# Optimization experiments

Measured on AMD Instinct MI355X. Metric: run time of the kernel, lower is better.

## Reference

```python
import jax, jax.numpy as jnp
import numpy as np
import math

B, T, D = 2, 2048, 2048
H, DH = 16, 128
DKV, DQ, DR = 512, 1024, 64
ROPE_BASE = 500000.0
EPS = 1e-6
SCALE = 1.0 / math.sqrt(DH + DR)


def setup_inputs() -> dict:
    key = jax.random.key(0)
    ks = jax.random.split(key, 12)
    s = 0.02
    return {
        'x': jax.random.normal(ks[0], (B, T, D), jnp.float32),
        'W_DQ': jax.random.normal(ks[1], (D, DQ), jnp.float32) * s,
        'W_UQ': jax.random.normal(ks[2], (DQ, H * DH), jnp.float32) * s,
        'W_QR': jax.random.normal(ks[3], (DQ, H * DR), jnp.float32) * s,
        'W_DKV': jax.random.normal(ks[4], (D, DKV), jnp.float32) * s,
        'W_UK': jax.random.normal(ks[5], (DKV, H * DH), jnp.float32) * s,
        'W_UV': jax.random.normal(ks[6], (DKV, H * DH), jnp.float32) * s,
        'W_KR': jax.random.normal(ks[7], (D, DR), jnp.float32) * s,
        'W_O': jax.random.normal(ks[8], (H * DH, D), jnp.float32) * s,
        'q_norm_w': jnp.ones((DQ,), jnp.float32),
        'kv_norm_w': jnp.ones((DKV,), jnp.float32),
    }


def _rmsnorm(v, w):
    n = jax.lax.rsqrt(jnp.mean(v * v, axis=-1, keepdims=True) + EPS)
    return v * n * w


def _rotate_half(v):
    v1, v2 = jnp.split(v, 2, axis=-1)
    return jnp.concatenate([-v2, v1], axis=-1)


def _rope_tables(seq_len):
    inv_freq = 1.0 / (ROPE_BASE ** (jnp.arange(0, DR, 2, dtype=jnp.float32) / DR))
    t = jnp.arange(seq_len, dtype=jnp.float32)
    freqs = jnp.outer(t, inv_freq)              # (S, DR/2)
    emb = jnp.concatenate([freqs, freqs], -1)   # (S, DR)
    return jnp.cos(emb), jnp.sin(emb)


def reference(x, W_DQ, W_UQ, W_QR, W_DKV, W_UK, W_UV, W_KR, W_O, q_norm_w, kv_norm_w):
    # Query path: low-rank compress -> RMSNorm -> up-project (content + rope parts)
    c_Q = _rmsnorm(x @ W_DQ, q_norm_w)                               # (B,T,DQ)
    q_C = (c_Q @ W_UQ).reshape(B, T, H, DH).transpose(0, 2, 1, 3)    # (B,H,T,DH)
    q_R = (c_Q @ W_QR).reshape(B, T, H, DR).transpose(0, 2, 1, 3)    # (B,H,T,DR)
    # KV path: joint low-rank latent + decoupled rope key
    c_KV = _rmsnorm(x @ W_DKV, kv_norm_w)                            # (B,T,DKV)
    k_C = (c_KV @ W_UK).reshape(B, T, H, DH).transpose(0, 2, 1, 3)   # (B,H,T,DH)
    v_C = (c_KV @ W_UV).reshape(B, T, H, DH).transpose(0, 2, 1, 3)   # (B,H,T,DH)
    k_R = (x @ W_KR)[:, None, :, :]                                  # (B,1,T,DR) shared across heads
    # Decoupled RoPE
    cos, sin = _rope_tables(T)
    cos = cos[None, None]; sin = sin[None, None]                     # (1,1,T,DR)
    q_R = q_R * cos + _rotate_half(q_R) * sin
    k_R = k_R * cos + _rotate_half(k_R) * sin
    k_R = jnp.broadcast_to(k_R, (B, H, T, DR))
    q = jnp.concatenate([q_C, q_R], axis=-1)                         # (B,H,T,DH+DR)
    k = jnp.concatenate([k_C, k_R], axis=-1)
    # Causal attention with MLA scale 1/sqrt(d_head + d_rope)
    scores = jnp.einsum('bhqd,bhkd->bhqk', q, k) * SCALE
    causal = jnp.tril(jnp.ones((T, T), bool))
    scores = jnp.where(causal, scores, jnp.finfo(scores.dtype).min)
    attn = jax.nn.softmax(scores, axis=-1)
    out = jnp.einsum('bhqk,bhkd->bhqd', attn, v_C)                   # (B,H,T,DH)
    out = out.transpose(0, 2, 1, 3).reshape(B, T, H * DH)
    return out @ W_O                                                 # (B,T,D)
```

## Files before the change

### kernel.cpp

```cpp
#include <hip/hip_runtime.h>
#include <cstdint>
#include <cstddef>

#define B_   2
#define T_   2048
#define D_   2048
#define H_   16
#define DH_  128
#define DQ_  1024
#define DKV_ 512
#define DR_  64
#define M_   4096
#define SCALE_ 0.07216878364870323f
#define SC2_   0.10412808709930322f
#define LN_BASE_ 13.122363377404328f

typedef unsigned short u16;
typedef __attribute__((ext_vector_type(8))) short short8;
typedef __attribute__((ext_vector_type(4))) float f32x4;

__device__ __forceinline__ float b2f(u16 u) { return __uint_as_float(((uint32_t)u) << 16); }
__device__ __forceinline__ u16 f2b(float f) {
    uint32_t x = __float_as_uint(f);
    return (u16)((x + 0x7fffu + ((x >> 16) & 1u)) >> 16);
}
__device__ __forceinline__ u16 f2b_fast(float f) {
    return (u16)((__float_as_uint(f) + 0x8000u) >> 16);
}

__device__ __forceinline__ void gload_lds16(const u16* src, u16* dst) {
    __builtin_amdgcn_global_load_lds(
        (const __attribute__((address_space(1))) uint32_t*)(uintptr_t)src,
        (__attribute__((address_space(3))) uint32_t*)(uintptr_t)dst, 16, 0, 0);
}

struct TPack {
    const float* src[8];
    u16*         dst[8];
    int K[8];
    int N[8];
    int ntx[8];
    int start[9];
};

__global__ __launch_bounds__(256) void prep_k(TPack p, const float* __restrict__ x,
                                              u16* __restrict__ xb, int ntr) {
    const int bid = blockIdx.x;
    if (bid < ntr) {
        __shared__ float tile[32][33];
        int w = 0;
#pragma unroll
        for (int i = 1; i < 8; ++i) if (bid >= p.start[i]) w = i;
        const int lt = bid - p.start[w];
        const int bx = lt % p.ntx[w], by = lt / p.ntx[w];
        const float* in = p.src[w];
        u16* out = p.dst[w];
        const int K = p.K[w], N = p.N[w];
        const int k0 = by * 32, n0 = bx * 32;
        const int tx = threadIdx.x & 31, ty = threadIdx.x >> 5;
#pragma unroll
        for (int i = 0; i < 4; ++i) {
            int k = k0 + ty + i * 8;
            int n = n0 + tx;
            tile[ty + i * 8][tx] = (n < N) ? in[(size_t)k * N + n] : 0.f;
        }
        __syncthreads();
#pragma unroll
        for (int i = 0; i < 4; ++i) {
            int n = n0 + ty + i * 8;
            out[(size_t)n * K + k0 + tx] = f2b(tile[tx][ty + i * 8]);
        }
    } else {
        const int i = ((bid - ntr) * 256 + threadIdx.x) * 4;
        const float4 v = *(const float4*)(x + i);
        ushort4 o;
        o.x = f2b(v.x); o.y = f2b(v.y); o.z = f2b(v.z); o.w = f2b(v.w);
        *(ushort4*)(xb + i) = o;
    }
}

template <int OUT_BF16>
__global__ __launch_bounds__(256) void gemm_tn(const u16* __restrict__ A,
                                               const u16* __restrict__ Bt,
                                               void* __restrict__ Cv,
                                               int N, int K) {
    __shared__ __attribute__((aligned(16))) u16 lA[128 * 32];
    __shared__ __attribute__((aligned(16))) u16 lB[128 * 32];
    const int m0 = blockIdx.y * 128, n0 = blockIdx.x * 128;
    const int tid = threadIdx.x, wave = tid >> 6, lane = tid & 63;
    const int wm = (wave >> 1) * 64, wn = (wave & 1) * 64;
    const int r = lane & 15, kq = lane >> 4;

    f32x4 acc[4][4];
#pragma unroll
    for (int i = 0; i < 4; ++i)
#pragma unroll
        for (int j = 0; j < 4; ++j) acc[i][j] = (f32x4){0.f, 0.f, 0.f, 0.f};

    for (int kk = 0; kk < K; kk += 32) {
#pragma unroll
        for (int p = 0; p < 2; ++p) {
            const int c = p * 256 + wave * 64 + lane;
            const u16* ga = A  + (size_t)(m0 + (c >> 2)) * K + kk + (c & 3) * 8;
            const u16* gb = Bt + (size_t)(n0 + (c >> 2)) * K + kk + (c & 3) * 8;
            u16* la = lA + (size_t)(p * 256 + wave * 64) * 8;
            u16* lb = lB + (size_t)(p * 256 + wave * 64) * 8;
            gload_lds16(ga, la);
            gload_lds16(gb, lb);
        }
        __syncthreads();
        short8 av[4], bv[4];
#pragma unroll
        for (int mi = 0; mi < 4; ++mi)
            av[mi] = *(const short8*)&lA[(wm + mi * 16 + r) * 32 + kq * 8];
#pragma unroll
        for (int ni = 0; ni < 4; ++ni)
            bv[ni] = *(const short8*)&lB[(wn + ni * 16 + r) * 32 + kq * 8];
#pragma unroll
        for (int mi = 0; mi < 4; ++mi)
#pragma unroll
            for (int ni = 0; ni < 4; ++ni)
                acc[mi][ni] = __builtin_amdgcn_mfma_f32_16x16x32_bf16(
                    av[mi], bv[ni], acc[mi][ni], 0, 0, 0);
        __syncthreads();
    }
    const int r4 = (lane >> 4) * 4, cc = lane & 15;
#pragma unroll
    for (int mi = 0; mi < 4; ++mi)
#pragma unroll
        for (int ni = 0; ni < 4; ++ni)
#pragma unroll
            for (int i = 0; i < 4; ++i) {
                const int row = m0 + wm + mi * 16 + r4 + i;
                const int col = n0 + wn + ni * 16 + cc;
                const float v = acc[mi][ni][i];
                if (OUT_BF16) ((u16*)Cv)[(size_t)row * N + col] = f2b(v);
                else          ((float*)Cv)[(size_t)row * N + col] = v;
            }
}

#define S_BM 256
#define S_BN 256
#define S_BK 64

__global__ __launch_bounds__(512, 1) void gemm256_k(const u16* __restrict__ A,
                                                    const u16* __restrict__ Bt,
                                                    u16* __restrict__ C,
                                                    int N, int K) {
    __shared__ __attribute__((aligned(16))) u16 sA[2][S_BM * S_BK];
    __shared__ __attribute__((aligned(16))) u16 sB[2][S_BN * S_BK];
    const int m0 = blockIdx.y * S_BM, n0 = blockIdx.x * S_BN;
    const int tid = threadIdx.x, lane = tid & 63;
    const int wave = tid >> 6;
    const int wm = wave >> 2, wn = wave & 3;
    const int r = lane & 15, kq = lane >> 4;

    const u16* gA[4]; const u16* gB[4]; int dOf[4];
#pragma unroll
    for (int is = 0; is < 4; ++is) {
        const int c = is * 512 + tid;
        const int row = c >> 3, c16 = c & 7;
        gA[is] = A  + (size_t)(m0 + row) * K + ((c16 ^ (row & 7)) * 8);
        gB[is] = Bt + (size_t)(n0 + row) * K + ((c16 ^ (row & 7)) * 8);
        dOf[is] = c * 8;
    }

    f32x4 acc[8][4];
#pragma unroll
    for (int i = 0; i < 8; ++i)
#pragma unroll
        for (int j = 0; j < 4; ++j) acc[i][j] = (f32x4){0.f, 0.f, 0.f, 0.f};

    const int NKT = K >> 6;

    auto STG = [&](int arr, int half, int bs, int kk) {
        u16* dst = arr ? (u16*)sB[bs] : (u16*)sA[bs];
        const u16** g = arr ? gB : gA;
#pragma unroll
        for (int is = half * 2; is < half * 2 + 2; ++is)
            gload_lds16(g[is] + kk, dst + dOf[is]);
    };

    STG(0, 0, 0, 0); STG(0, 1, 0, 0); STG(1, 0, 0, 0); STG(1, 1, 0, 0);

    short8 af[4][2], bf[2][2];
    for (int kt = 0; kt < NKT; ++kt) {
        const int cur = kt & 1;
        const int kk = (kt + 1) * 64;
        const int pf = (kt + 1 < NKT);
        const u16* cA = sA[cur];
        const u16* cB = sB[cur];

        auto lda = [&](int row, int g) -> short8 {
            return *(const short8*)&cA[row * 64 + ((g ^ (row & 7)) * 8)];
        };
        auto ldb = [&](int row, int g) -> short8 {
            return *(const short8*)&cB[row * 64 + ((g ^ (row & 7)) * 8)];
        };

#pragma unroll
        for (int ph = 0; ph < 4; ++ph) {
            const int mh = ph >> 1;
            const int nh = (ph == 1 || ph == 2) ? 1 : 0;
            if (pf) STG(ph >> 1, ph & 1, cur ^ 1, kk);
            if (ph == 0) {
                if (pf) asm volatile("s_waitcnt vmcnt(2)" ::: "memory");
                else    asm volatile("s_waitcnt vmcnt(0)" ::: "memory");
            }
            __builtin_amdgcn_s_barrier();
            asm volatile("" ::: "memory");
            if (!(ph & 1)) {
#pragma unroll
                for (int mi = 0; mi < 4; ++mi)
#pragma unroll
                    for (int ks = 0; ks < 2; ++ks)
                        af[mi][ks] = lda(wm * 128 + mh * 64 + mi * 16 + r, ks * 4 + kq);
            }
#pragma unroll
            for (int ni = 0; ni < 2; ++ni)
#pragma unroll
                for (int ks = 0; ks < 2; ++ks)
                    bf[ni][ks] = ldb(wn * 64 + nh * 32 + ni * 16 + r, ks * 4 + kq);
#pragma unroll
            for (int ks = 0; ks < 2; ++ks)
#pragma unroll
                for (int mi = 0; mi < 4; ++mi)
#pragma unroll
                    for (int ni = 0; ni < 2; ++ni)
                        acc[mh * 4 + mi][nh * 2 + ni] =
                            __builtin_amdgcn_mfma_f32_16x16x32_bf16(
                                af[mi][ks], bf[ni][ks],
                                acc[mh * 4 + mi][nh * 2 + ni], 0, 0, 0);
            asm volatile("" ::: "memory");
            __builtin_amdgcn_s_barrier();
            asm volatile("" ::: "memory");
        }
    }

    const int r4c = kq * 4, cc = lane & 15;
#pragma unroll
    for (int mf = 0; mf < 8; ++mf)
#pragma unroll
        for (int nf = 0; nf < 4; ++nf)
#pragma unroll
            for (int i = 0; i < 4; ++i) {
                const int row = m0 + wm * 128 + mf * 16 + r4c + i;
                const int col = n0 + wn * 64 + nf * 16 + cc;
                C[(size_t)row * N + col] = f2b(acc[mf][nf][i]);
            }
}

__global__ __launch_bounds__(256) void normrope_k(const u16* __restrict__ P1,
                                                  const float* __restrict__ qnw,
                                                  const float* __restrict__ kvnw,
                                                  u16* __restrict__ cQb,
                                                  u16* __restrict__ cKVb,
                                                  u16* __restrict__ kRb) {
    const int which = blockIdx.y;
    if (which < 2) {
        const int row = blockIdx.x;
        const int N = which ? 512 : 1024;
        const int off = which ? 1024 : 0;
        const float* w = which ? kvnw : qnw;
        u16* outp = which ? cKVb : cQb;
        const u16* src = P1 + (size_t)row * 1664 + off;
        const int j = threadIdx.x * 4;
        float v[4] = {0.f, 0.f, 0.f, 0.f};
        if (j < N) {
            ushort4 u = *(const ushort4*)(src + j);
            v[0] = b2f(u.x); v[1] = b2f(u.y); v[2] = b2f(u.z); v[3] = b2f(u.w);
        }
        float ss = v[0]*v[0] + v[1]*v[1] + v[2]*v[2] + v[3]*v[3];
#pragma unroll
        for (int offc = 32; offc; offc >>= 1) ss += __shfl_down(ss, offc);
        __shared__ float red[4];
        const int wave = threadIdx.x >> 6, lane = threadIdx.x & 63;
        if (lane == 0) red[wave] = ss;
        __syncthreads();
        const float tot = red[0] + red[1] + red[2] + red[3];
        const float sc = rsqrtf(tot / (float)N + 1e-6f);
        if (j < N) {
            ushort4 o;
            o.x = f2b(v[0] * sc * w[j]);
            o.y = f2b(v[1] * sc * w[j + 1]);
            o.z = f2b(v[2] * sc * w[j + 2]);
            o.w = f2b(v[3] * sc * w[j + 3]);
            *(ushort4*)(outp + (size_t)row * N + j) = o;
        }
    } else {
        if (blockIdx.x >= 1024) return;
        const int row = blockIdx.x * 4 + (threadIdx.x >> 6);
        const int j = threadIdx.x & 63;
        const int t = row & (T_ - 1);
        const int i = j & 31;
        const float invf = __expf(-LN_BASE_ * (float)(2 * i) * (1.0f / 64.0f));
        const float ang = (float)t * invf;
        const float c = cosf(ang), s = sinf(ang);
        const u16* src = P1 + (size_t)row * 1664 + 1536;
        const float v = b2f(src[j]);
        const float rot = (j < 32) ? -b2f(src[j + 32]) : b2f(src[j - 32]);
        kRb[(size_t)row * 64 + j] = f2b(v * c + rot * s);
    }
}

__global__ __launch_bounds__(256) void vtrans_k(const u16* __restrict__ P3,
                                                u16* __restrict__ Vt) {
    __shared__ u16 tile[64][72];
    const int tt = blockIdx.x;
    const int b = tt >> 10;
    const int rem = tt & 1023;
    const int by = rem >> 5, bx = rem & 31;
    const int t0 = by * 64, c0 = bx * 64;
    const int tid = threadIdx.x;
    const int rr2 = tid >> 3;
    const int c8 = tid & 7;
#pragma unroll
    for (int p = 0; p < 2; ++p) {
        const int row = p * 32 + rr2;
        *(uint4*)&tile[row][c8 * 8] =
            *(const uint4*)(P3 + (size_t)(b * T_ + t0 + row) * 4096 + 2048 + c0 + c8 * 8);
    }
    __syncthreads();
#pragma unroll
    for (int p = 0; p < 2; ++p) {
        const int c = p * 32 + rr2;
        u16 tmp[8];
#pragma unroll
        for (int j = 0; j < 8; ++j) tmp[j] = tile[c8 * 8 + j][c];
        *(uint4*)(Vt + ((size_t)b * 2048 + c0 + c) * 2048 + t0 + c8 * 8) = *(uint4*)tmp;
    }
}

#define ABQ  128
#define ABK  64
#define NW   8
#define KSTR 200
#define VSTR 72
#define PSTR 72
#define VOFF 12800
#define KVSZ 22016
#define QSTRIDE 3072
#define KSTRIDE 4096

__global__ __launch_bounds__(512, 1) void attn_mfma_k(
    const u16* __restrict__ qC,
    const u16* __restrict__ kC, const u16* __restrict__ kR,
    const u16* __restrict__ Vt, u16* __restrict__ outp)
{
    __shared__ __attribute__((aligned(16))) u16 sKV[3][KVSZ];
    __shared__ __attribute__((aligned(16))) u16 sP[NW * 16 * PSTR];

    const int h = blockIdx.x, b = blockIdx.z;
    const int qb = b ? (15 - (int)blockIdx.y) : (int)blockIdx.y;
    const int q0 = qb * ABQ;
    const int tid = threadIdx.x, wave = tid >> 6, lane = tid & 63;
    const int r = lane & 15, kq = lane >> 4, r4 = kq * 4;
    const int wq = wave * 16;

    const u16* gsrc[6]; int gstep[6]; int doff[6];
#pragma unroll
    for (int j = 0; j < 6; ++j) {
        const int i = wave + NW * j;
        const int slot = (i < 43) ? i : (i - 43);
        if (slot < 25) {
            const int s = slot * 64 + lane;
            const int rr2 = s / 25;
            int cc = s - rr2 * 25;
            if (cc > 23) cc = 0;
            if (cc < 16) {
                gsrc[j] = kC + (size_t)(b * T_ + rr2) * KSTRIDE + h * 128 + cc * 8;
                gstep[j] = ABK * KSTRIDE;
            } else {
                gsrc[j] = kR + (size_t)(b * T_ + rr2) * 64 + (cc - 16) * 8;
                gstep[j] = ABK * 64;
            }
            doff[j] = slot * 512;
        } else {
            const int sl = slot - 25;
            const int s = sl * 64 + lane;
            const int rr2 = s / 9;
            int cc = s - rr2 * 9;
            if (cc > 7) cc = 0;
            gsrc[j] = Vt + ((size_t)(b * H_ + h) * 128 + rr2) * T_ + cc * 8;
            gstep[j] = ABK;
            doff[j] = VOFF + sl * 512;
        }
    }

    short8 qf[6];
    {
        const int t = q0 + wq + r;
        const u16* qcrow = qC + (size_t)(b * T_ + t) * QSTRIDE + h * 128 + kq * 8;
#pragma unroll
        for (int kc = 0; kc < 4; ++kc) qf[kc] = *(const short8*)(qcrow + kc * 32);
        const u16* qrraw = qC + (size_t)(b * T_ + t) * QSTRIDE + 2048 + h * 64 + kq * 8;
        const short8 q0v = *(const short8*)(qrraw);
        const short8 q1v = *(const short8*)(qrraw + 32);
        short8 o0, o1;
#pragma unroll
        for (int j = 0; j < 8; ++j) {
            const int i = kq * 8 + j;
            const float invf = __expf(-LN_BASE_ * (float)(2 * i) * (1.0f / 64.0f));
            const float ang = (float)t * invf;
            const float cs = cosf(ang), sn = sinf(ang);
            const float a = b2f((u16)q0v[j]), bb = b2f((u16)q1v[j]);
            o0[j] = (short)f2b(a * cs - bb * sn);
            o1[j] = (short)f2b(bb * cs + a * sn);
        }
        qf[4] = o0; qf[5] = o1;
    }

    f32x4 Oa[8];
#pragma unroll
    for (int nt = 0; nt < 8; ++nt) Oa[nt] = (f32x4){0.f, 0.f, 0.f, 0.f};
    float Lrow[4] = {0.f, 0.f, 0.f, 0.f};

    u16* myP = sP + wave * 16 * PSTR;

    auto STAGE = [&](int kt2, int bs) {
        u16* dst = &sKV[bs][0];
#pragma unroll
        for (int j = 0; j < 6; ++j)
            gload_lds16(gsrc[j] + (size_t)kt2 * (size_t)gstep[j], dst + doff[j]);
    };

    const int nkt = 2 * qb + 2;
    STAGE(0, 0);
    STAGE(1, 1);
    for (int kt = 0; kt < nkt; ++kt) {
        const int cur = kt % 3;
        if (kt == 0 || kt >= nkt - 1) {
            asm volatile("s_waitcnt vmcnt(0)" ::: "memory");
        } else {
            asm volatile("s_waitcnt vmcnt(6)" ::: "memory");
        }
        __builtin_amdgcn_s_barrier();
        asm volatile("" ::: "memory");

        const u16* cK = &sKV[cur][0];
        const u16* cV = &sKV[cur][VOFF];
        const int k0 = kt * ABK;

        f32x4 Sa[4];
#pragma unroll
        for (int nt = 0; nt < 4; ++nt) Sa[nt] = (f32x4){0.f, 0.f, 0.f, 0.f};
#pragma unroll
        for (int kc = 0; kc < 6; ++kc) {
            short8 kf[4];
#pragma unroll
            for (int nt = 0; nt < 4; ++nt)
                kf[nt] = *(const short8*)&cK[(nt * 16 + r) * KSTR + (kc * 4 + kq) * 8];
#pragma unroll
            for (int nt = 0; nt < 4; ++nt)
                Sa[nt] = __builtin_amdgcn_mfma_f32_16x16x32_bf16(
                    qf[kc], kf[nt], Sa[nt], 0, 0, 0);
        }

        if (kt < nkt - 2) {
#pragma unroll
            for (int i = 0; i < 4; ++i) {
                float sm = 0.f;
#pragma unroll
                for (int nt = 0; nt < 4; ++nt) {
                    const float p = exp2f(Sa[nt][i] * SC2_);
                    sm += p;
                    myP[(r4 + i) * PSTR + nt * 16 + r] = f2b_fast(p);
                }
                Lrow[i] += sm;
            }
        } else {
#pragma unroll
            for (int i = 0; i < 4; ++i) {
                const int grow = q0 + wq + r4 + i;
                float sm = 0.f;
#pragma unroll
                for (int nt = 0; nt < 4; ++nt) {
                    float p = exp2f(Sa[nt][i] * SC2_);
                    p = (k0 + nt * 16 + r > grow) ? 0.f : p;
                    sm += p;
                    myP[(r4 + i) * PSTR + nt * 16 + r] = f2b_fast(p);
                }
                Lrow[i] += sm;
            }
        }

#pragma unroll
        for (int kc2 = 0; kc2 < 2; ++kc2) {
            const short8 pf = *(const short8*)&myP[r * PSTR + (kc2 * 4 + kq) * 8];
#pragma unroll
            for (int nt = 0; nt < 8; ++nt) {
                const short8 vf = *(const short8*)&cV[(nt * 16 + r) * VSTR + (kc2 * 4 + kq) * 8];
                Oa[nt] = __builtin_amdgcn_mfma_f32_16x16x32_bf16(
                    pf, vf, Oa[nt], 0, 0, 0);
            }
        }

        if (kt + 2 < nkt) STAGE(kt + 2, (kt + 2) % 3);
    }

#pragma unroll
    for (int i = 0; i < 4; ++i) {
        float L = Lrow[i];
        L += __shfl_xor(L, 1);
        L += __shfl_xor(L, 2);
        L += __shfl_xor(L, 4);
        L += __shfl_xor(L, 8);
        const float inv = 1.0f / L;
        const int t = q0 + wq + r4 + i;
        u16* orow = outp + (size_t)(b * T_ + t) * 2048 + h * 128;
#pragma unroll
        for (int nt = 0; nt < 8; ++nt)
            orow[nt * 16 + r] = f2b(Oa[nt][i] * inv);
    }
}

extern "C" void kernel_launch(void* const* d_in, const int* in_sizes, int n_in,
                              void* d_out, int out_size, void* d_ws, size_t ws_size,
                              hipStream_t stream) {
    (void)in_sizes; (void)n_in; (void)out_size; (void)ws_size;
    const float* x     = (const float*)d_in[0];
    const float* W_DQ  = (const float*)d_in[1];
    const float* W_UQ  = (const float*)d_in[2];
    const float* W_QR  = (const float*)d_in[3];
    const float* W_DKV = (const float*)d_in[4];
    const float* W_UK  = (const float*)d_in[5];
    const float* W_UV  = (const float*)d_in[6];
    const float* W_KR  = (const float*)d_in[7];
    const float* W_O   = (const float*)d_in[8];
    const float* qnw   = (const float*)d_in[9];
    const float* kvnw  = (const float*)d_in[10];
    float* out = (float*)d_out;

    char* base = (char*)d_ws;
    size_t o = 0;
    auto alloc = [&](size_t bytes) {
        char* r = base + o;
        o += (bytes + 255) & ~(size_t)255;
        return r;
    };
    u16* WT1  = (u16*)alloc((size_t)1664 * 2048 * 2);
    u16* WT2  = (u16*)alloc((size_t)3072 * 1024 * 2);
    u16* WT3  = (u16*)alloc((size_t)4096 * 512 * 2);
    u16* WT_O = (u16*)alloc((size_t)2048 * 2048 * 2);
    u16* xb   = (u16*)alloc((size_t)M_ * 2048 * 2);
    u16* U1   = (u16*)alloc((size_t)M_ * 2048 * 2);
    u16* P2   = (u16*)alloc((size_t)M_ * 3072 * 2);
    u16* P3   = (u16*)alloc((size_t)M_ * 4096 * 2);
    u16* cQb  = (u16*)alloc((size_t)M_ * 1024 * 2);
    u16* cKVb = (u16*)alloc((size_t)M_ * 512 * 2);
    u16* qRb  = (u16*)alloc((size_t)M_ * 1024 * 2);
    u16* kRb  = (u16*)alloc((size_t)M_ * 64 * 2);
    (void)qRb;
    u16* P1       = U1;
    u16* attn_out = U1;
    u16* Vt       = xb;

    TPack tp;
    const float* srcs[8] = {W_DQ, W_DKV, W_KR, W_UQ, W_QR, W_UK, W_UV, W_O};
    u16* dsts[8] = {WT1, WT1 + (size_t)1024*2048, WT1 + (size_t)1536*2048,
                    WT2, WT2 + (size_t)2048*1024,
                    WT3, WT3 + (size_t)2048*512, WT_O};
    const int Ks[8]   = {2048, 2048, 2048, 1024, 1024, 512, 512, 2048};
    const int Ns[8]   = {1024,  512,   64, 2048, 1024, 2048, 2048, 2048};
    const int ntxs[8] = {  32,   16,    4,   64,   32,   64,   64,   64};
    int cum = 0;
    for (int i = 0; i < 8; ++i) {
        tp.src[i] = srcs[i]; tp.dst[i] = dsts[i];
        tp.K[i] = Ks[i]; tp.N[i] = Ns[i]; tp.ntx[i] = ntxs[i];
        tp.start[i] = cum;
        cum += ntxs[i] * (Ks[i] / 32);
    }
    tp.start[8] = cum;
    const int ncast = (M_ * D_) / 1024;
    prep_k<<<cum + ncast, 256, 0, stream>>>(tp, x, xb, cum);

    gemm_tn<1><<<dim3(1664/128, M_/128), 256, 0, stream>>>(xb, WT1, (void*)P1, 1664, 2048);

    normrope_k<<<dim3(M_, 3), 256, 0, stream>>>(P1, qnw, kvnw, cQb, cKVb, kRb);

    gemm_tn<1><<<dim3(3072/128, M_/128), 256, 0, stream>>>(cQb, WT2, (void*)P2, 3072, 1024);

    gemm256_k<<<dim3(4096/256, M_/256), 512, 0, stream>>>(cKVb, WT3, P3, 4096, 512);

    vtrans_k<<<2048, 256, 0, stream>>>(P3, Vt);

    attn_mfma_k<<<dim3(H_, T_/ABQ, B_), 512, 0, stream>>>(P2, P3, kRb, Vt, attn_out);

    gemm_tn<0><<<dim3(2048/128, M_/128), 256, 0, stream>>>(attn_out, WT_O, (void*)out, 2048, 2048);
}
```

Before: 396.7 us.

## Merge Q and KV up-projection GEMMs, fuse V transpose, use 256-tile output GEMM

Puts the cQ up-projection and the cKV up-projection into one grouped launch built on a shared 256x256 GEMM core. Blocks covering the V columns write their results transposed straight into Vt, so the separate transpose kernel goes away. The final output projection also moves from the 128-tile GEMM to the 256-tile core with fp32 stores. This cuts launches and the extra V read/write pass, but the transposed stores are narrow (4-element) and scattered, and the output GEMM now runs only 128 blocks.

```diff
diff --git a/kernel.cpp b/kernel.cpp
--- a/kernel.cpp
+++ b/kernel.cpp
@@ -143,17 +143,15 @@
 #define S_BN 256
 #define S_BK 64
 
-__global__ __launch_bounds__(512, 1) void gemm256_k(const u16* __restrict__ A,
-                                                    const u16* __restrict__ Bt,
-                                                    u16* __restrict__ C,
-                                                    int N, int K) {
-    __shared__ __attribute__((aligned(16))) u16 sA[2][S_BM * S_BK];
-    __shared__ __attribute__((aligned(16))) u16 sB[2][S_BN * S_BK];
-    const int m0 = blockIdx.y * S_BM, n0 = blockIdx.x * S_BN;
-    const int tid = threadIdx.x, lane = tid & 63;
+__device__ __forceinline__ void gemm256_core(
+    const u16* __restrict__ A, const u16* __restrict__ Bt, int K,
+    int m0, int n0, int tid, f32x4 (&acc)[8][4],
+    u16 (*sA)[S_BM * S_BK], u16 (*sB)[S_BN * S_BK]) {
+    const int lane = tid & 63;
     const int wave = tid >> 6;
-    const int wm = wave >> 2, wn = wave & 3;
+    const int wm = wave >> 2;
     const int r = lane & 15, kq = lane >> 4;
+    const int wn = wave & 3;
 
     const u16* gA[4]; const u16* gB[4]; int dOf[4];
 #pragma unroll
@@ -164,12 +162,6 @@
         gB[is] = Bt + (size_t)(n0 + row) * K + ((c16 ^ (row & 7)) * 8);
         dOf[is] = c * 8;
     }
-
-    f32x4 acc[8][4];
-#pragma unroll
-    for (int i = 0; i < 8; ++i)
-#pragma unroll
-        for (int j = 0; j < 4; ++j) acc[i][j] = (f32x4){0.f, 0.f, 0.f, 0.f};
 
     const int NKT = K >> 6;
 
@@ -236,6 +228,92 @@
             asm volatile("" ::: "memory");
         }
     }
+}
+
+__global__ __launch_bounds__(512, 1) void gemm256p_k(
+    const u16* __restrict__ A0, const u16* __restrict__ B0,
+    u16* __restrict__ C0, int N0c, int K0,
+    const u16* __restrict__ A1, const u16* __restrict__ B1,
+    u16* __restrict__ C1, int N1c, int K1,
+    u16* __restrict__ Vt, int vcol0, int nx0)
+{
+    __shared__ __attribute__((aligned(16))) u16 sA[2][S_BM * S_BK];
+    __shared__ __attribute__((aligned(16))) u16 sB[2][S_BN * S_BK];
+    const int sel = (int)blockIdx.x >= nx0;
+    const u16* A  = sel ? A1 : A0;
+    const u16* Bt = sel ? B1 : B0;
+    const int  K  = sel ? K1 : K0;
+    const int lbx = sel ? (blockIdx.x - nx0) : blockIdx.x;
+    const int m0 = blockIdx.y * S_BM, n0 = lbx * S_BN;
+    const int tid = threadIdx.x, lane = tid & 63;
+    const int wave = tid >> 6, wm = wave >> 2, wn = wave & 3;
+    const int kq = lane >> 4;
+
+    f32x4 acc[8][4];
+#pragma unroll
+    for (int i = 0; i < 8; ++i)
+#pragma unroll
+        for (int j = 0; j < 4; ++j) acc[i][j] = (f32x4){0.f, 0.f, 0.f, 0.f};
+
+    gemm256_core(A, Bt, K, m0, n0, tid, acc, sA, sB);
+
+    const int r4c = kq * 4, cc = lane & 15;
+    if (!sel) {
+#pragma unroll
+        for (int mf = 0; mf < 8; ++mf)
+#pragma unroll
+            for (int nf = 0; nf < 4; ++nf)
+#pragma unroll
+                for (int i = 0; i < 4; ++i) {
+                    const int row = m0 + wm * 128 + mf * 16 + r4c + i;
+                    const int col = n0 + wn * 64 + nf * 16 + cc;
+                    C0[(size_t)row * N0c + col] = f2b(acc[mf][nf][i]);
+                }
+    } else if (n0 < vcol0) {
+#pragma unroll
+        for (int mf = 0; mf < 8; ++mf)
+#pragma unroll
+            for (int nf = 0; nf < 4; ++nf)
+#pragma unroll
+                for (int i = 0; i < 4; ++i) {
+                    const int row = m0 + wm * 128 + mf * 16 + r4c + i;
+                    const int col = n0 + wn * 64 + nf * 16 + cc;
+                    C1[(size_t)row * N1c + col] = f2b(acc[mf][nf][i]);
+                }
+    } else {
+#pragma unroll
+        for (int mf = 0; mf < 8; ++mf)
+#pragma unroll
+            for (int nf = 0; nf < 4; ++nf) {
+                const int tp = m0 + wm * 128 + mf * 16 + r4c;
+                const int c  = n0 - vcol0 + wn * 64 + nf * 16 + cc;
+                u16 tmp[4];
+#pragma unroll
+                for (int i = 0; i < 4; ++i) tmp[i] = f2b(acc[mf][nf][i]);
+                *(ushort4*)&Vt[((size_t)((tp >> 11) * 2048 + c)) * 2048 + (tp & 2047)]
+                    = *(ushort4*)tmp;
+            }
+    }
+}
+
+__global__ __launch_bounds__(512, 1) void gemm256o_k(
+    const u16* __restrict__ A, const u16* __restrict__ Bt,
+    float* __restrict__ Cf, int N, int K)
+{
+    __shared__ __attribute__((aligned(16))) u16 sA[2][S_BM * S_BK];
+    __shared__ __attribute__((aligned(16))) u16 sB[2][S_BN * S_BK];
+    const int m0 = blockIdx.y * S_BM, n0 = blockIdx.x * S_BN;
+    const int tid = threadIdx.x, lane = tid & 63;
+    const int wave = tid >> 6, wm = wave >> 2, wn = wave & 3;
+    const int kq = lane >> 4;
+
+    f32x4 acc[8][4];
+#pragma unroll
+    for (int i = 0; i < 8; ++i)
+#pragma unroll
+        for (int j = 0; j < 4; ++j) acc[i][j] = (f32x4){0.f, 0.f, 0.f, 0.f};
+
+    gemm256_core(A, Bt, K, m0, n0, tid, acc, sA, sB);
 
     const int r4c = kq * 4, cc = lane & 15;
 #pragma unroll
@@ -246,7 +324,7 @@
             for (int i = 0; i < 4; ++i) {
                 const int row = m0 + wm * 128 + mf * 16 + r4c + i;
                 const int col = n0 + wn * 64 + nf * 16 + cc;
-                C[(size_t)row * N + col] = f2b(acc[mf][nf][i]);
+                Cf[(size_t)row * N + col] = acc[mf][nf][i];
             }
 }
 
@@ -300,34 +378,6 @@
         const float v = b2f(src[j]);
         const float rot = (j < 32) ? -b2f(src[j + 32]) : b2f(src[j - 32]);
         kRb[(size_t)row * 64 + j] = f2b(v * c + rot * s);
-    }
-}
-
-__global__ __launch_bounds__(256) void vtrans_k(const u16* __restrict__ P3,
-                                                u16* __restrict__ Vt) {
-    __shared__ u16 tile[64][72];
-    const int tt = blockIdx.x;
-    const int b = tt >> 10;
-    const int rem = tt & 1023;
-    const int by = rem >> 5, bx = rem & 31;
-    const int t0 = by * 64, c0 = bx * 64;
-    const int tid = threadIdx.x;
-    const int rr2 = tid >> 3;
-    const int c8 = tid & 7;
-#pragma unroll
-    for (int p = 0; p < 2; ++p) {
-        const int row = p * 32 + rr2;
-        *(uint4*)&tile[row][c8 * 8] =
-            *(const uint4*)(P3 + (size_t)(b * T_ + t0 + row) * 4096 + 2048 + c0 + c8 * 8);
-    }
-    __syncthreads();
-#pragma unroll
-    for (int p = 0; p < 2; ++p) {
-        const int c = p * 32 + rr2;
-        u16 tmp[8];
-#pragma unroll
-        for (int j = 0; j < 8; ++j) tmp[j] = tile[c8 * 8 + j][c];
-        *(uint4*)(Vt + ((size_t)b * 2048 + c0 + c) * 2048 + t0 + c8 * 8) = *(uint4*)tmp;
     }
 }
 
@@ -578,13 +628,12 @@
 
     normrope_k<<<dim3(M_, 3), 256, 0, stream>>>(P1, qnw, kvnw, cQb, cKVb, kRb);
 
-    gemm_tn<1><<<dim3(3072/128, M_/128), 256, 0, stream>>>(cQb, WT2, (void*)P2, 3072, 1024);
-
-    gemm256_k<<<dim3(4096/256, M_/256), 512, 0, stream>>>(cKVb, WT3, P3, 4096, 512);
-
-    vtrans_k<<<2048, 256, 0, stream>>>(P3, Vt);
+    gemm256p_k<<<dim3(3072/256 + 4096/256, M_/256), 512, 0, stream>>>(
+        cQb,  WT2, P2, 3072, 1024,
+        cKVb, WT3, P3, 4096, 512,
+        Vt, 2048, 3072/256);
 
     attn_mfma_k<<<dim3(H_, T_/ABQ, B_), 512, 0, stream>>>(P2, P3, kRb, Vt, attn_out);
 
-    gemm_tn<0><<<dim3(2048/128, M_/128), 256, 0, stream>>>(attn_out, WT_O, (void*)out, 2048, 2048);
-}
+    gemm256o_k<<<dim3(2048/256, M_/256), 512, 0, stream>>>(attn_out, WT_O, out, 2048, 2048);
+}
```

Result: no change. 391.5 us (-1.3%).
